# Performance work log

Hardware: AMD Instinct MI355X
Metric: run time of the kernel (lower is better)

Reference implementation:

```python
import jax, jax.numpy as jnp
import numpy as np

DIM = 1024
DIM_LATENT = 1024
DIM_HEAD = 64
INNER = max(DIM, DIM_LATENT)  # 1024
HEADS = INNER // DIM_HEAD     # 16
SCALE = DIM_HEAD ** -0.5
LN_EPS = 1e-5
RMS_EPS = 1e-8


def layernorm(x, g, b):
    mu = jnp.mean(x, axis=-1, keepdims=True)
    var = jnp.mean(jnp.square(x - mu), axis=-1, keepdims=True)
    return (x - mu) * jax.lax.rsqrt(var + LN_EPS) * g + b


def rmsnorm(x, gamma):
    # torch: x / clamp(norm(x,-1) * d**-0.5, eps) * gamma
    n = jnp.linalg.norm(x, axis=-1, keepdims=True) * (x.shape[-1] ** -0.5)
    return x / jnp.maximum(n, RMS_EPS) * gamma


def setup_inputs() -> dict:
    key = jax.random.key(0)
    ks = jax.random.split(key, 8)
    b, n, nl = 8, 2048, 512
    x = jax.random.normal(ks[0], (b, n, DIM), dtype=jnp.float32)
    latents = jax.random.normal(ks[1], (b, nl, DIM_LATENT), dtype=jnp.float32)
    mask = jax.random.randint(ks[2], (b, n), 0, 2).astype(bool)
    init = lambda k, shape, fan_in: jax.random.normal(k, shape, jnp.float32) * (fan_in ** -0.5)
    return {
        "x": x,
        "latents": latents,
        "mask": mask,
        "ln_x_g": jnp.ones((DIM,), jnp.float32),
        "ln_x_b": jnp.zeros((DIM,), jnp.float32),
        "ln_l_g": jnp.ones((DIM_LATENT,), jnp.float32),
        "ln_l_b": jnp.zeros((DIM_LATENT,), jnp.float32),
        "q_gamma": jnp.ones((DIM_HEAD,), jnp.float32),
        "k_gamma": jnp.ones((DIM_HEAD,), jnp.float32),
        "W_q": init(ks[3], (DIM_LATENT, INNER), DIM_LATENT),
        "W_kv": init(ks[4], (DIM, 2 * INNER), DIM),
        "W_out": init(ks[5], (INNER, DIM_LATENT), INNER),
        "b_out": jnp.zeros((DIM_LATENT,), jnp.float32),
    }


def reference(x, latents, mask, ln_x_g, ln_x_b, ln_l_g, ln_l_b,
              q_gamma, k_gamma, W_q, W_kv, W_out, b_out):
    b, n, _ = x.shape
    nl = latents.shape[1]
    xn = layernorm(x, ln_x_g, ln_x_b)
    ln = layernorm(latents, ln_l_g, ln_l_b)

    q = ln @ W_q                                   # [b, nl, inner]
    kv = jnp.concatenate([xn @ W_kv, ln @ W_kv], axis=1)  # [b, n+nl, 2*inner]
    k, v = kv[..., :INNER], kv[..., INNER:]

    to_heads = lambda t: t.reshape(t.shape[0], t.shape[1], HEADS, DIM_HEAD).transpose(0, 2, 1, 3)
    q, k, v = to_heads(q), to_heads(k), to_heads(v)  # [b, h, *, d]

    qn = rmsnorm(q, q_gamma) * SCALE
    kn = rmsnorm(k, k_gamma)

    sim = jnp.einsum('bhid,bhjd->bhij', qn, kn)      # [b, h, nl, n+nl]
    full_mask = jnp.pad(mask, ((0, 0), (0, nl)), constant_values=True)
    neg = -jnp.finfo(sim.dtype).max
    sim = jnp.where(full_mask[:, None, None, :], sim, neg)

    attn = jax.nn.softmax(sim.astype(jnp.float32), axis=-1).astype(sim.dtype)
    out = jnp.einsum('bhij,bhjd->bhid', attn, v)     # [b, h, nl, d]
    out = out.transpose(0, 2, 1, 3).reshape(b, nl, INNER)
    return out @ W_out + b_out
```

## Files before the change

kernel.cpp:

```cpp
#include <hip/hip_runtime.h>
#include <hip/hip_bf16.h>
#include <cfloat>
#include <cmath>

typedef __hip_bfloat16 bf16;
#define DEV_INLINE __device__ __forceinline__

typedef __attribute__((ext_vector_type(8))) short short8;
typedef __attribute__((ext_vector_type(4))) short short4v;
typedef __attribute__((ext_vector_type(4))) float float4v;
typedef __attribute__((ext_vector_type(16))) float float16v;

#define BATCH 8
#define NSEQ 2048
#define NLAT 512
#define DIM_ 1024
#define NKV 2560
#define HEADS_ 16
#define DHEAD 64
#define SCALE_ 0.125f
#define LN_EPS_ 1e-5f
#define RMS_EPS_ 1e-8f

DEV_INLINE float bf2f(bf16 v) { return __bfloat162float(v); }
DEV_INLINE bf16 f2bf(float v) { return __float2bfloat16(v); }
DEV_INLINE short bfbits(float x) { union { bf16 b; short s; } c; c.b = f2bf(x); return c.s; }
DEV_INLINE float sbits2f(short s) { union { bf16 b; short s; } c; c.s = s; return bf2f(c.b); }

DEV_INLINE int detect_bf16(const void* ones) {
    return (*(const unsigned*)ones == 0x3F803F80u) ? 1 : 0;
}

template<typename T> DEV_INLINE float ldf(const T* p);
template<> DEV_INLINE float ldf<float>(const float* p) { return *p; }
template<> DEV_INLINE float ldf<bf16>(const bf16* p)  { return __bfloat162float(*p); }

DEV_INLINE void gload16(const bf16* g, bf16* l) {
    __builtin_amdgcn_global_load_lds(
        (const __attribute__((address_space(1))) unsigned int*)g,
        (__attribute__((address_space(3))) unsigned int*)l,
        16, 0, 0);
}

DEV_INLINE float block_sum_256(float v, float* sred) {
    #pragma unroll
    for (int o = 1; o < 64; o <<= 1) v += __shfl_xor(v, o, 64);
    int w = threadIdx.x >> 6;
    __syncthreads();
    if ((threadIdx.x & 63) == 0) sred[w] = v;
    __syncthreads();
    return sred[0] + sred[1] + sred[2] + sred[3];
}

template<typename T>
DEV_INLINE void ln_row_body(int r, const void* xv, const void* latv,
                            const void* gxv, const void* bxv,
                            const void* glv, const void* blv,
                            bf16* __restrict__ out, float* sred)
{
    const T* src; const T* g; const T* be; bf16* o;
    if (r < BATCH * NSEQ) {
        int b = r >> 11, i = r & 2047;
        src = (const T*)xv + (size_t)r * DIM_;
        o = out + ((size_t)b * NKV + i) * DIM_;
        g = (const T*)gxv; be = (const T*)bxv;
    } else {
        int rr = r - BATCH * NSEQ;
        int b = rr >> 9, i = rr & 511;
        src = (const T*)latv + (size_t)rr * DIM_;
        o = out + ((size_t)b * NKV + NSEQ + i) * DIM_;
        g = (const T*)glv; be = (const T*)blv;
    }
    int t = threadIdx.x;
    float v[4];
    float s = 0.f;
    #pragma unroll
    for (int j = 0; j < 4; j++) { v[j] = ldf(src + t + j * 256); s += v[j]; }
    s = block_sum_256(s, sred);
    float mu = s * (1.f / 1024.f);
    float s2 = 0.f;
    #pragma unroll
    for (int j = 0; j < 4; j++) { float d = v[j] - mu; s2 += d * d; }
    s2 = block_sum_256(s2, sred);
    float rstd = rsqrtf(s2 * (1.f / 1024.f) + LN_EPS_);
    #pragma unroll
    for (int j = 0; j < 4; j++) {
        int c = t + j * 256;
        o[c] = f2bf((v[j] - mu) * rstd * ldf(g + c) + ldf(be + c));
    }
}

template<typename T>
DEV_INLINE void trans_body(int bid, const void* wqv, const void* wkvv, const void* woutv,
                           bf16* wqT, bf16* wkvT, bf16* woutT, float* tile )
{
    const T* in; bf16* out; int N, t0;
    if (bid < 1024)      { in = (const T*)wqv;   out = wqT;   N = 1024; t0 = bid; }
    else if (bid < 3072) { in = (const T*)wkvv;  out = wkvT;  N = 2048; t0 = bid - 1024; }
    else                 { in = (const T*)woutv; out = woutT; N = 1024; t0 = bid - 3072; }
    int K = 1024;
    int nb = N >> 5;
    int bn = (t0 % nb) * 32, bk = (t0 / nb) * 32;
    int tx = threadIdx.x & 31, ty = threadIdx.x >> 5;
    #pragma unroll
    for (int j = 0; j < 4; j++)
        tile[(ty + j * 8) * 33 + tx] = ldf(in + (size_t)(bk + ty + j * 8) * N + bn + tx);
    __syncthreads();
    #pragma unroll
    for (int j = 0; j < 4; j++)
        out[(size_t)(bn + ty + j * 8) * K + bk + tx] = f2bf(tile[tx * 33 + ty + j * 8]);
}

__global__ __launch_bounds__(256) void prep_kernel(
    const void* x, const void* lat,
    const void* gx, const void* bx, const void* gl, const void* bl,
    const void* wq, const void* wkv, const void* wout,
    bf16* __restrict__ cat_n, bf16* __restrict__ wqT,
    bf16* __restrict__ wkvT, bf16* __restrict__ woutT)
{
    __shared__ float smem[32 * 33];
    int isb = detect_bf16(gx);
    int bid = blockIdx.x;
    if (bid < 20480) {
        if (isb) ln_row_body<bf16>(bid, x, lat, gx, bx, gl, bl, cat_n, smem);
        else     ln_row_body<float>(bid, x, lat, gx, bx, gl, bl, cat_n, smem);
    } else {
        int t = bid - 20480;
        if (isb) trans_body<bf16>(t, wq, wkv, wout, wqT, wkvT, woutT, smem);
        else     trans_body<float>(t, wq, wkv, wout, wqT, wkvT, woutT, smem);
    }
}

#define MFMA_CORE_128(As, Bs, Apt, Bpt, K, acc)                                \
    {                                                                          \
        bf16* Asl_ = &As[threadIdx.x * 8];                                     \
        bf16* Bsl_ = &Bs[threadIdx.x * 8];                                     \
        for (int k0 = 0; k0 < K; k0 += 64) {                                   \
            __syncthreads();                                                   \
            _Pragma("unroll")                                                  \
            for (int rep = 0; rep < 4; rep++) {                                \
                gload16(Apt[rep] + k0, Asl_ + rep * 2048);                     \
                gload16(Bpt[rep] + k0, Bsl_ + rep * 2048);                     \
            }                                                                  \
            __syncthreads();                                                   \
            _Pragma("unroll")                                                  \
            for (int kk = 0; kk < 4; kk++) {                                   \
                short8 af_[2], bf_[2];                                         \
                _Pragma("unroll")                                              \
                for (int ms = 0; ms < 2; ms++) {                               \
                    int row = wm * 64 + ms * 32 + l32;                         \
                    int jc = (kk * 2 + h5) ^ (row & 7);                        \
                    af_[ms] = *(const short8*)&As[row * 64 + jc * 8];          \
                }                                                              \
                _Pragma("unroll")                                              \
                for (int ns = 0; ns < 2; ns++) {                               \
                    int row = wn * 64 + ns * 32 + l32;                         \
                    int jc = (kk * 2 + h5) ^ (row & 7);                        \
                    bf_[ns] = *(const short8*)&Bs[row * 64 + jc * 8];          \
                }                                                              \
                _Pragma("unroll")                                              \
                for (int ms = 0; ms < 2; ms++)                                 \
                    _Pragma("unroll")                                          \
                    for (int ns = 0; ns < 2; ns++)                             \
                        acc[ms][ns] = __builtin_amdgcn_mfma_f32_32x32x16_bf16( \
                            af_[ms], bf_[ns], acc[ms][ns], 0, 0, 0);           \
            }                                                                  \
        }                                                                      \
    }

#define QKV_MFMA2(BQ0, BQ1, NB)                                               \
    __builtin_amdgcn_s_barrier(); asm volatile("" ::: "memory");              \
    __builtin_amdgcn_s_setprio(1);                                            \
    _Pragma("unroll")                                                         \
    for (int m_ = 0; m_ < 8; m_++) {                                          \
        acc[m_][NB] = __builtin_amdgcn_mfma_f32_16x16x32_bf16(                \
            af[m_], BQ0, acc[m_][NB], 0, 0, 0);                               \
        acc[m_][NB + 1] = __builtin_amdgcn_mfma_f32_16x16x32_bf16(            \
            af[m_], BQ1, acc[m_][NB + 1], 0, 0, 0);                           \
    }                                                                         \
    __builtin_amdgcn_s_setprio(0);                                            \
    __builtin_amdgcn_s_barrier(); asm volatile("" ::: "memory");

__global__ __launch_bounds__(512, 2) void gemm_qkv(
    const void* gq, const void* gk,
    const bf16* __restrict__ cat_n, const bf16* __restrict__ wkvT,
    const bf16* __restrict__ wqT,
    bf16* __restrict__ kbuf, bf16* __restrict__ vtbuf, bf16* __restrict__ qbuf)
{
    __shared__ bf16 S[8][8192];
    int isb = detect_bf16(gq);
    int tid = threadIdx.x;
    int bid = blockIdx.x;
    int lane = tid & 63;
    int l16 = lane & 15, quad = lane >> 4;
    int wv = tid >> 6;
    int wm = wv >> 2, wn = wv & 3;

    int x = bid & 7, ii = bid >> 3;
    int bm, bn; bool isq; const bf16* Bt;
    if (ii < 80) { bm = (ii >> 3) * 8 + x; bn = ii & 7; Bt = wkvT; isq = false; }
    else { int j = ii - 80; bm = (j >> 2) * 8 + x; bn = j & 3; Bt = wqT; isq = true; }

    int r0 = tid >> 2;
    int c0 = (tid & 3) ^ ((r0 >> 1) & 3);
    int r1 = (tid + 512) >> 2;
    int c1 = (tid & 3) ^ ((r1 >> 1) & 3);
    int ar0 = bm * 256 + r0, ar1 = bm * 256 + r1;
    size_t ga0 = isq ? ((size_t)(ar0 >> 9) * NKV + NSEQ + (ar0 & 511)) : (size_t)ar0;
    size_t ga1 = isq ? ((size_t)(ar1 >> 9) * NKV + NSEQ + (ar1 & 511)) : (size_t)ar1;
    const bf16* pA0 = cat_n + ga0 * 1024 + c0 * 8;
    const bf16* pA1 = cat_n + ga1 * 1024 + c1 * 8;
    const bf16* pB0 = Bt + (size_t)(bn * 256 + r0) * 1024 + c0 * 8;
    const bf16* pB1 = Bt + (size_t)(bn * 256 + r1) * 1024 + c1 * 8;

#define STG(P0, P1, SLOT, KO) do {                                            \
        gload16((P0) + (KO), &S[SLOT][0] + tid * 8);                          \
        gload16((P1) + (KO), &S[SLOT][0] + 4096 + tid * 8);                   \
    } while (0)

    int qx = (quad ^ ((l16 >> 1) & 3)) * 8;
    int aoff = (wm * 128 + l16) * 32 + qx;
    int boff = (wn * 64 + l16) * 32 + qx;

    float4v acc[8][4];
    #pragma unroll
    for (int m = 0; m < 8; m++)
        #pragma unroll
        for (int n = 0; n < 4; n++)
            #pragma unroll
            for (int r = 0; r < 4; r++) acc[m][n][r] = 0.f;

    STG(pA0, pA1, 0, 0);
    STG(pB0, pB1, 2, 0);
    STG(pA0, pA1, 1, 32);
    STG(pB0, pB1, 3, 32);
    STG(pA0, pA1, 4, 64);
    STG(pB0, pB1, 6, 64);
    asm volatile("s_waitcnt vmcnt(4)" ::: "memory");
    __builtin_amdgcn_s_barrier(); asm volatile("" ::: "memory");

    short8 af[8], b0[4], b1[4];
    b0[0] = *(const short8*)&S[2][boff];
    b0[1] = *(const short8*)&S[2][boff + 512];

    for (int t = 0; t < 16; ++t) {
        int cur = (t & 1) * 4, nxt = cur ^ 4;
        const bf16* A0k = &S[cur + 0][0];
        const bf16* A1k = &S[cur + 1][0];
        const bf16* B0k = &S[cur + 2][0];
        const bf16* B1k = &S[cur + 3][0];
        const bf16* Bn0 = &S[nxt + 2][0];
        int ko1 = t * 64 + 96;
        int ko2 = t * 64 + 128;

        #pragma unroll
        for (int m = 0; m < 8; m++) af[m] = *(const short8*)&A0k[aoff + m * 512];
        if (t < 15) STG(pA0, pA1, nxt + 1, ko1);
        QKV_MFMA2(b0[0], b0[1], 0)

        b0[2] = *(const short8*)&B0k[boff + 1024];
        b0[3] = *(const short8*)&B0k[boff + 1536];
        b1[0] = *(const short8*)&B1k[boff];
        b1[1] = *(const short8*)&B1k[boff + 512];
        if (t < 15) STG(pB0, pB1, nxt + 3, ko1);
        QKV_MFMA2(b0[2], b0[3], 2)

        #pragma unroll
        for (int m = 0; m < 8; m++) af[m] = *(const short8*)&A1k[aoff + m * 512];
        if (t < 14) STG(pA0, pA1, cur + 0, ko2);
        QKV_MFMA2(b1[0], b1[1], 0)

        b1[2] = *(const short8*)&B1k[boff + 1024];
        b1[3] = *(const short8*)&B1k[boff + 1536];
        if (t < 14) {
            STG(pB0, pB1, cur + 2, ko2);
            asm volatile("s_waitcnt vmcnt(4)" ::: "memory");
        } else {
            asm volatile("s_waitcnt vmcnt(0)" ::: "memory");
        }
        if (t < 15) {
            b0[0] = *(const short8*)&Bn0[boff];
            b0[1] = *(const short8*)&Bn0[boff + 512];
        }
        QKV_MFMA2(b1[2], b1[3], 2)
    }
#undef STG

    if (isq || bn < 4) {
        const void* gp = isq ? gq : gk;
        float g2[4];
        #pragma unroll
        for (int n = 0; n < 4; n++) {
            int idx = n * 16 + l16;
            g2[n] = isb ? bf2f(((const bf16*)gp)[idx]) : ((const float*)gp)[idx];
        }
        #pragma unroll
        for (int m = 0; m < 8; m++) {
            #pragma unroll
            for (int r = 0; r < 4; r++) {
                float ss = acc[m][0][r] * acc[m][0][r]
                         + acc[m][1][r] * acc[m][1][r]
                         + acc[m][2][r] * acc[m][2][r]
                         + acc[m][3][r] * acc[m][3][r];
                ss += __shfl_xor(ss, 1, 64);
                ss += __shfl_xor(ss, 2, 64);
                ss += __shfl_xor(ss, 4, 64);
                ss += __shfl_xor(ss, 8, 64);
                float nn = sqrtf(ss) * 0.125f;
                float inv = 1.0f / fmaxf(nn, RMS_EPS_);
                if (isq) inv *= SCALE_;
                #pragma unroll
                for (int n = 0; n < 4; n++) acc[m][n][r] *= inv * g2[n];
            }
        }
    }

    if (!isq && bn >= 4) {
        int bq_ = bm / 10;
        int key0 = (bm % 10) * 256 + wm * 128;
        #pragma unroll
        for (int m = 0; m < 8; m++) {
            int key = key0 + m * 16 + quad * 4;
            #pragma unroll
            for (int n = 0; n < 4; n++) {
                int col = bn * 256 + wn * 64 + n * 16 + l16 - 1024;
                int h = col >> 6, d = col & 63;
                short4v ov;
                #pragma unroll
                for (int r = 0; r < 4; r++) ov[r] = bfbits(acc[m][n][r]);
                *(short4v*)(vtbuf + ((size_t)((bq_ * 16 + h) * 64 + d)) * NKV + key) = ov;
            }
        }
    } else {
        bf16* C = isq ? qbuf : kbuf;
        int rbase = bm * 256 + wm * 128;
        int cbase = bn * 256 + wn * 64;
        #pragma unroll
        for (int m = 0; m < 8; m++) {
            #pragma unroll
            for (int r = 0; r < 4; r++) {
                int row = rbase + m * 16 + quad * 4 + r;
                #pragma unroll
                for (int n = 0; n < 4; n++)
                    C[(size_t)row * 1024 + cbase + n * 16 + l16] = f2bf(acc[m][n][r]);
            }
        }
    }
}

#define KC 64
__global__ __launch_bounds__(256) void attn_mfma(
    const bf16* __restrict__ q, const bf16* __restrict__ kbuf,
    const bf16* __restrict__ vtbuf, const int* __restrict__ maskp,
    const void* gk, bf16* __restrict__ out)
{
    __shared__ bf16 Ks[KC * 64];
    __shared__ bf16 Vt[DHEAD * 64];
    __shared__ bf16 Ps[4][2][16][64];
    __shared__ float msk_s[KC];

    int isb = detect_bf16(gk);
    int tid = threadIdx.x;
    int bid = blockIdx.x;
    int bh = bid & 127, qb = bid >> 7;
    int h = bh & 15, bb = bh >> 4;
    int wv = tid >> 6, lane = tid & 63, quad = lane >> 4, l16 = lane & 15;
    int q8 = quad * 8;
    int qbase = qb * 128 + wv * 32;
    int sw = l16 & 7;

    const bf16* kbase = kbuf + (size_t)bb * NKV * 1024 + h * DHEAD;
    const bf16* vbase = vtbuf + (size_t)(bb * 16 + h) * DHEAD * NKV;

    short8 qf[2][2];
    #pragma unroll
    for (int qt = 0; qt < 2; qt++) {
        const bf16* qp = q + ((size_t)(bb * NLAT + qbase + qt * 16 + l16)) * 1024 + h * DHEAD;
        qf[qt][0] = *(const short8*)(qp + q8);
        qf[qt][1] = *(const short8*)(qp + q8 + 32);
    }

    float gv = isb ? bf2f(((const bf16*)gk)[lane]) : ((const float*)gk)[lane];
    gv = fabsf(gv);
    #pragma unroll
    for (int o = 1; o < 64; o <<= 1) gv = fmaxf(gv, __shfl_xor(gv, o, 64));
    float m_fix[2];
    #pragma unroll
    for (int qt = 0; qt < 2; qt++) {
        float ssq = 0.f;
        #pragma unroll
        for (int j = 0; j < 8; j++) {
            float a = sbits2f(qf[qt][0][j]);
            float b = sbits2f(qf[qt][1][j]);
            ssq += a * a + b * b;
        }
        ssq += __shfl_xor(ssq, 16, 64);
        ssq += __shfl_xor(ssq, 32, 64);
        m_fix[qt] = sqrtf(ssq) * 8.0f * gv;
    }

    int c0 = tid, c1 = tid + 256;
    int krow0 = c0 >> 3, kj0 = ((c0 & 7) ^ (krow0 & 7)) * 8;
    int krow1 = c1 >> 3, kj1 = ((c1 & 7) ^ (krow1 & 7)) * 8;

    float4v o_acc[2][4];
    #pragma unroll
    for (int qt = 0; qt < 2; qt++)
        #pragma unroll
        for (int ds = 0; ds < 4; ds++)
            #pragma unroll
            for (int r = 0; r < 4; r++) o_acc[qt][ds][r] = 0.f;
    float l_i[2] = {0.f, 0.f};

    for (int kb = 0; kb < NKV; kb += KC) {
        __syncthreads();
        gload16(kbase + (size_t)(kb + krow0) * 1024 + kj0, &Ks[c0 * 8]);
        gload16(kbase + (size_t)(kb + krow1) * 1024 + kj1, &Ks[c1 * 8]);
        gload16(vbase + (size_t)krow0 * NKV + kb + kj0, &Vt[c0 * 8]);
        gload16(vbase + (size_t)krow1 * NKV + kb + kj1, &Vt[c1 * 8]);
        if (tid < KC) {
            int key = kb + tid;
            float mv = 0.f;
            if (key < NSEQ) mv = maskp[bb * NSEQ + key] ? 0.f : -1e30f;
            msk_s[tid] = mv;
        }
        __syncthreads();

        float4v st[2][4];
        #pragma unroll
        for (int kt = 0; kt < 4; kt++) {
            int row = kt * 16 + l16;
            short8 kf0 = *(const short8*)&Ks[row * 64 + ((quad ^ sw) << 3)];
            short8 kf1 = *(const short8*)&Ks[row * 64 + (((quad + 4) ^ sw) << 3)];
            #pragma unroll
            for (int qt = 0; qt < 2; qt++) {
                float4v z; z[0]=0.f; z[1]=0.f; z[2]=0.f; z[3]=0.f;
                z = __builtin_amdgcn_mfma_f32_16x16x32_bf16(kf0, qf[qt][0], z, 0, 0, 0);
                z = __builtin_amdgcn_mfma_f32_16x16x32_bf16(kf1, qf[qt][1], z, 0, 0, 0);
                st[qt][kt] = z;
            }
        }
        float4 mv4[4];
        #pragma unroll
        for (int kt = 0; kt < 4; kt++) mv4[kt] = *(const float4*)&msk_s[kt * 16 + 4 * quad];
        #pragma unroll
        for (int qt = 0; qt < 2; qt++) {
            float lp = 0.f;
            #pragma unroll
            for (int kt = 0; kt < 4; kt++) {
                const float* mk = (const float*)&mv4[kt];
                short4v pk;
                #pragma unroll
                for (int r = 0; r < 4; r++) {
                    float e = __expf(st[qt][kt][r] + mk[r] - m_fix[qt]);
                    lp += e;
                    pk[r] = bfbits(e);
                }
                int j = kt * 2 + (quad >> 1);
                int js = j ^ sw;
                *(short4v*)&Ps[wv][qt][l16][js * 8 + (quad & 1) * 4] = pk;
            }
            l_i[qt] += lp;
        }

        #pragma unroll
        for (int kc = 0; kc < 2; kc++) {
            short8 pf[2];
            #pragma unroll
            for (int qt = 0; qt < 2; qt++)
                pf[qt] = *(const short8*)&Ps[wv][qt][l16][((kc * 4 + quad) ^ sw) * 8];
            #pragma unroll
            for (int ds = 0; ds < 4; ds++) {
                int row = ds * 16 + l16;
                short8 vf = *(const short8*)&Vt[row * 64 + (((kc * 4 + quad) ^ sw) << 3)];
                #pragma unroll
                for (int qt = 0; qt < 2; qt++)
                    o_acc[qt][ds] = __builtin_amdgcn_mfma_f32_16x16x32_bf16(vf, pf[qt], o_acc[qt][ds], 0, 0, 0);
            }
        }
    }

    #pragma unroll
    for (int qt = 0; qt < 2; qt++) {
        float l = l_i[qt];
        l += __shfl_xor(l, 16, 64);
        l += __shfl_xor(l, 32, 64);
        float inv = 1.0f / l;
        bf16* op = out + ((size_t)(bb * NLAT + qbase + qt * 16 + l16)) * 1024 + h * DHEAD;
        #pragma unroll
        for (int ds = 0; ds < 4; ds++) {
            short4v ov;
            #pragma unroll
            for (int r = 0; r < 4; r++) ov[r] = bfbits(o_acc[qt][ds][r] * inv);
            *(short4v*)(op + ds * 16 + 4 * quad) = ov;
        }
    }
}

__global__ __launch_bounds__(256) void gemm_out(
    const void* ones, const void* bias,
    const bf16* __restrict__ A, const bf16* __restrict__ Bt, void* __restrict__ Cout)
{
    __shared__ bf16 As[128 * 64];
    __shared__ bf16 Bs[128 * 64];
    int isb = detect_bf16(ones);

    int tid = threadIdx.x;
    int bid = blockIdx.x;
    int bm = (bid >> 6) * 8 + (bid & 7);
    int bn = (bid >> 3) & 7;
    int wv = tid >> 6, lane = tid & 63, l32 = lane & 31, h5 = lane >> 5;
    int wm = wv >> 1, wn = wv & 1;
    const int K = 1024, N = 1024;

    const bf16* Apt[4]; const bf16* Bpt[4];
    #pragma unroll
    for (int rep = 0; rep < 4; rep++) {
        int c = rep * 256 + tid;
        int row = c >> 3;
        int k8 = ((c & 7) ^ (row & 7)) * 8;
        Apt[rep] = A + (size_t)(bm * 128 + row) * K + k8;
        Bpt[rep] = Bt + (size_t)(bn * 128 + row) * K + k8;
    }

    float16v acc[2][2];
    #pragma unroll
    for (int i = 0; i < 2; i++)
        #pragma unroll
        for (int j = 0; j < 2; j++)
            #pragma unroll
            for (int r = 0; r < 16; r++) acc[i][j][r] = 0.f;

    MFMA_CORE_128(As, Bs, Apt, Bpt, K, acc);

    #pragma unroll
    for (int ms = 0; ms < 2; ms++) {
        #pragma unroll
        for (int rg = 0; rg < 4; rg++) {
            int row0 = bm * 128 + wm * 64 + ms * 32 + rg * 8 + h5 * 4;
            #pragma unroll
            for (int rr = 0; rr < 4; rr++) {
                int row = row0 + rr;
                #pragma unroll
                for (int ns = 0; ns < 2; ns++) {
                    int col = bn * 128 + wn * 64 + ns * 32 + l32;
                    float bv = isb ? bf2f(((const bf16*)bias)[col]) : ((const float*)bias)[col];
                    float v = acc[ms][ns][rg * 4 + rr] + bv;
                    if (isb) ((bf16*)Cout)[(size_t)row * N + col] = f2bf(v);
                    else     ((float*)Cout)[(size_t)row * N + col] = v;
                }
            }
        }
    }
}

extern "C" void kernel_launch(void* const* d_in, const int* in_sizes, int n_in,
                              void* d_out, int out_size, void* d_ws, size_t ws_size,
                              hipStream_t stream) {
    const int* mask = (const int*)d_in[2];

    char* ws = (char*)d_ws;
    size_t off = 0;
    bf16* cat_n   = (bf16*)(ws + off); off += (size_t)20480 * 1024 * 2;
    bf16* kbuf    = (bf16*)(ws + off); off += (size_t)20480 * 1024 * 2;
    bf16* vtbuf   = (bf16*)(ws + off); off += (size_t)8192 * 2560 * 2;
    bf16* qbuf    = (bf16*)(ws + off); off += (size_t)4096 * 1024 * 2;
    bf16* attnout = (bf16*)(ws + off); off += (size_t)4096 * 1024 * 2;
    bf16* wqT     = (bf16*)(ws + off); off += (size_t)1024 * 1024 * 2;
    bf16* wkvT    = (bf16*)(ws + off); off += (size_t)2048 * 1024 * 2;
    bf16* woutT   = (bf16*)(ws + off); off += (size_t)1024 * 1024 * 2;

    prep_kernel<<<24576, 256, 0, stream>>>(
        d_in[0], d_in[1], d_in[3], d_in[4], d_in[5], d_in[6],
        d_in[9], d_in[10], d_in[11], cat_n, wqT, wkvT, woutT);

    gemm_qkv<<<704, 512, 0, stream>>>(
        d_in[7], d_in[8], cat_n, wkvT, wqT, kbuf, vtbuf, qbuf);

    attn_mfma<<<512, 256, 0, stream>>>(qbuf, kbuf, vtbuf, mask, d_in[8], attnout);

    gemm_out<<<256, 256, 0, stream>>>(
        d_in[3], d_in[12], attnout, woutT, d_out);
}
```

Measured before the change: 357.5 us.

## Double-buffer K/V tiles in attention, preload mask, restructure QKV MFMA clusters

The attention kernel now double-buffers the K and V shared-memory tiles, issuing the next tile's global loads before computing on the current one, and drops one barrier per iteration. The full mask row is converted into shared memory once up front instead of per tile. The QKV GEMM loads all four B fragments at once and runs two larger MFMA clusters per k-step, with an explicit lgkmcnt wait and sched_barrier, instead of four smaller interleaved ones. This uses more LDS and registers and makes the waits coarser, so it could lower occupancy or expose LDS latency.

```diff
diff --git a/kernel.cpp b/kernel.cpp
--- a/kernel.cpp
+++ b/kernel.cpp
@@ -168,16 +168,17 @@
         }                                                                      \
     }
 
-#define QKV_MFMA2(BQ0, BQ1, NB)                                               \
+#define QKV_CLUSTER()                                                         \
     __builtin_amdgcn_s_barrier(); asm volatile("" ::: "memory");              \
+    asm volatile("s_waitcnt lgkmcnt(0)" ::: "memory");                        \
+    __builtin_amdgcn_sched_barrier(0);                                        \
     __builtin_amdgcn_s_setprio(1);                                            \
     _Pragma("unroll")                                                         \
-    for (int m_ = 0; m_ < 8; m_++) {                                          \
-        acc[m_][NB] = __builtin_amdgcn_mfma_f32_16x16x32_bf16(                \
-            af[m_], BQ0, acc[m_][NB], 0, 0, 0);                               \
-        acc[m_][NB + 1] = __builtin_amdgcn_mfma_f32_16x16x32_bf16(            \
-            af[m_], BQ1, acc[m_][NB + 1], 0, 0, 0);                           \
-    }                                                                         \
+    for (int m_ = 0; m_ < 8; m_++)                                            \
+        _Pragma("unroll")                                                     \
+        for (int n_ = 0; n_ < 4; n_++)                                        \
+            acc[m_][n_] = __builtin_amdgcn_mfma_f32_16x16x32_bf16(            \
+                af[m_], bfr[n_], acc[m_][n_], 0, 0, 0);                       \
     __builtin_amdgcn_s_setprio(0);                                            \
     __builtin_amdgcn_s_barrier(); asm volatile("" ::: "memory");
 
@@ -239,50 +240,38 @@
     asm volatile("s_waitcnt vmcnt(4)" ::: "memory");
     __builtin_amdgcn_s_barrier(); asm volatile("" ::: "memory");
 
-    short8 af[8], b0[4], b1[4];
-    b0[0] = *(const short8*)&S[2][boff];
-    b0[1] = *(const short8*)&S[2][boff + 512];
-
+    short8 af[8], bfr[4];
     for (int t = 0; t < 16; ++t) {
         int cur = (t & 1) * 4, nxt = cur ^ 4;
         const bf16* A0k = &S[cur + 0][0];
         const bf16* A1k = &S[cur + 1][0];
         const bf16* B0k = &S[cur + 2][0];
         const bf16* B1k = &S[cur + 3][0];
-        const bf16* Bn0 = &S[nxt + 2][0];
         int ko1 = t * 64 + 96;
         int ko2 = t * 64 + 128;
 
         #pragma unroll
         for (int m = 0; m < 8; m++) af[m] = *(const short8*)&A0k[aoff + m * 512];
-        if (t < 15) STG(pA0, pA1, nxt + 1, ko1);
-        QKV_MFMA2(b0[0], b0[1], 0)
-
-        b0[2] = *(const short8*)&B0k[boff + 1024];
-        b0[3] = *(const short8*)&B0k[boff + 1536];
-        b1[0] = *(const short8*)&B1k[boff];
-        b1[1] = *(const short8*)&B1k[boff + 512];
-        if (t < 15) STG(pB0, pB1, nxt + 3, ko1);
-        QKV_MFMA2(b0[2], b0[3], 2)
+        #pragma unroll
+        for (int n = 0; n < 4; n++) bfr[n] = *(const short8*)&B0k[boff + n * 512];
+        if (t < 15) {
+            STG(pA0, pA1, nxt + 1, ko1);
+            STG(pB0, pB1, nxt + 3, ko1);
+        }
+        QKV_CLUSTER()
 
         #pragma unroll
         for (int m = 0; m < 8; m++) af[m] = *(const short8*)&A1k[aoff + m * 512];
-        if (t < 14) STG(pA0, pA1, cur + 0, ko2);
-        QKV_MFMA2(b1[0], b1[1], 0)
-
-        b1[2] = *(const short8*)&B1k[boff + 1024];
-        b1[3] = *(const short8*)&B1k[boff + 1536];
+        #pragma unroll
+        for (int n = 0; n < 4; n++) bfr[n] = *(const short8*)&B1k[boff + n * 512];
         if (t < 14) {
+            STG(pA0, pA1, cur + 0, ko2);
             STG(pB0, pB1, cur + 2, ko2);
             asm volatile("s_waitcnt vmcnt(4)" ::: "memory");
         } else {
             asm volatile("s_waitcnt vmcnt(0)" ::: "memory");
         }
-        if (t < 15) {
-            b0[0] = *(const short8*)&Bn0[boff];
-            b0[1] = *(const short8*)&Bn0[boff + 512];
-        }
-        QKV_MFMA2(b1[2], b1[3], 2)
+        QKV_CLUSTER()
     }
 #undef STG
 
@@ -354,10 +343,10 @@
     const bf16* __restrict__ vtbuf, const int* __restrict__ maskp,
     const void* gk, bf16* __restrict__ out)
 {
-    __shared__ bf16 Ks[KC * 64];
-    __shared__ bf16 Vt[DHEAD * 64];
+    __shared__ bf16 Ks[2][KC * 64];
+    __shared__ bf16 Vt[2][DHEAD * 64];
     __shared__ bf16 Ps[4][2][16][64];
-    __shared__ float msk_s[KC];
+    __shared__ float msk_all[NSEQ];
 
     int isb = detect_bf16(gk);
     int tid = threadIdx.x;
@@ -372,6 +361,12 @@
     const bf16* kbase = kbuf + (size_t)bb * NKV * 1024 + h * DHEAD;
     const bf16* vbase = vtbuf + (size_t)(bb * 16 + h) * DHEAD * NKV;
 
+    #pragma unroll
+    for (int j = 0; j < 8; j++) {
+        int key = j * 256 + tid;
+        msk_all[key] = maskp[bb * NSEQ + key] ? 0.f : -1e30f;
+    }
+
     short8 qf[2][2];
     #pragma unroll
     for (int qt = 0; qt < 2; qt++) {
@@ -399,9 +394,16 @@
         m_fix[qt] = sqrtf(ssq) * 8.0f * gv;
     }
 
-    int c0 = tid, c1 = tid + 256;
-    int krow0 = c0 >> 3, kj0 = ((c0 & 7) ^ (krow0 & 7)) * 8;
-    int krow1 = c1 >> 3, kj1 = ((c1 & 7) ^ (krow1 & 7)) * 8;
+    int sc0 = tid, sc1 = tid + 256;
+    int krow0 = sc0 >> 3, kj0 = ((sc0 & 7) ^ (krow0 & 7)) * 8;
+    int krow1 = sc1 >> 3, kj1 = ((sc1 & 7) ^ (krow1 & 7)) * 8;
+
+#define ASTG(B, KB) do {                                                      \
+        gload16(kbase + (size_t)((KB) + krow0) * 1024 + kj0, &Ks[B][sc0 * 8]);\
+        gload16(kbase + (size_t)((KB) + krow1) * 1024 + kj1, &Ks[B][sc1 * 8]);\
+        gload16(vbase + (size_t)krow0 * NKV + (KB) + kj0, &Vt[B][sc0 * 8]);   \
+        gload16(vbase + (size_t)krow1 * NKV + (KB) + kj1, &Vt[B][sc1 * 8]);   \
+    } while (0)
 
     float4v o_acc[2][4];
     #pragma unroll
@@ -412,26 +414,19 @@
             for (int r = 0; r < 4; r++) o_acc[qt][ds][r] = 0.f;
     float l_i[2] = {0.f, 0.f};
 
+    ASTG(0, 0);
+    __syncthreads();
+
+    int buf = 0;
     for (int kb = 0; kb < NKV; kb += KC) {
-        __syncthreads();
-        gload16(kbase + (size_t)(kb + krow0) * 1024 + kj0, &Ks[c0 * 8]);
-        gload16(kbase + (size_t)(kb + krow1) * 1024 + kj1, &Ks[c1 * 8]);
-        gload16(vbase + (size_t)krow0 * NKV + kb + kj0, &Vt[c0 * 8]);
-        gload16(vbase + (size_t)krow1 * NKV + kb + kj1, &Vt[c1 * 8]);
-        if (tid < KC) {
-            int key = kb + tid;
-            float mv = 0.f;
-            if (key < NSEQ) mv = maskp[bb * NSEQ + key] ? 0.f : -1e30f;
-            msk_s[tid] = mv;
-        }
-        __syncthreads();
+        if (kb + KC < NKV) ASTG(buf ^ 1, kb + KC);
 
         float4v st[2][4];
         #pragma unroll
         for (int kt = 0; kt < 4; kt++) {
             int row = kt * 16 + l16;
-            short8 kf0 = *(const short8*)&Ks[row * 64 + ((quad ^ sw) << 3)];
-            short8 kf1 = *(const short8*)&Ks[row * 64 + (((quad + 4) ^ sw) << 3)];
+            short8 kf0 = *(const short8*)&Ks[buf][row * 64 + ((quad ^ sw) << 3)];
+            short8 kf1 = *(const short8*)&Ks[buf][row * 64 + (((quad + 4) ^ sw) << 3)];
             #pragma unroll
             for (int qt = 0; qt < 2; qt++) {
                 float4v z; z[0]=0.f; z[1]=0.f; z[2]=0.f; z[3]=0.f;
@@ -441,8 +436,15 @@
             }
         }
         float4 mv4[4];
-        #pragma unroll
-        for (int kt = 0; kt < 4; kt++) mv4[kt] = *(const float4*)&msk_s[kt * 16 + 4 * quad];
+        if (kb < NSEQ) {
+            #pragma unroll
+            for (int kt = 0; kt < 4; kt++)
+                mv4[kt] = *(const float4*)&msk_all[kb + kt * 16 + 4 * quad];
+        } else {
+            #pragma unroll
+            for (int kt = 0; kt < 4; kt++)
+                mv4[kt] = make_float4(0.f, 0.f, 0.f, 0.f);
+        }
         #pragma unroll
         for (int qt = 0; qt < 2; qt++) {
             float lp = 0.f;
@@ -472,13 +474,17 @@
             #pragma unroll
             for (int ds = 0; ds < 4; ds++) {
                 int row = ds * 16 + l16;
-                short8 vf = *(const short8*)&Vt[row * 64 + (((kc * 4 + quad) ^ sw) << 3)];
+                short8 vf = *(const short8*)&Vt[buf][row * 64 + (((kc * 4 + quad) ^ sw) << 3)];
                 #pragma unroll
                 for (int qt = 0; qt < 2; qt++)
                     o_acc[qt][ds] = __builtin_amdgcn_mfma_f32_16x16x32_bf16(vf, pf[qt], o_acc[qt][ds], 0, 0, 0);
             }
         }
-    }
+
+        __syncthreads();
+        buf ^= 1;
+    }
+#undef ASTG
 
     #pragma unroll
     for (int qt = 0; qt < 2; qt++) {
```

New measurement: 370.5 us. 1.04x slower.

## Switch QKV GEMM to 32x32x16 MFMA with simpler double-buffered pipeline

Applied to the files above, without the earlier changes.

The QKV projection GEMM moves from 16x16x32 MFMA tiles to 32x32x16 MFMA tiles, so each wave holds a 4x2 grid of 16-float accumulators instead of 8x4 float4s. The staggered four-phase prefetch with partial vmcnt waits and barriers around every MFMA group is replaced by a plain double buffer: prefetch the whole next k-tile, compute both halves, then wait and barrier once per iteration. The RMSNorm and store epilogues are remapped to the new accumulator layout, adding one more shuffle step. Larger MFMAs reduce LDS fragment reads per FLOP, but the simpler pipeline may expose more global-load latency.

```diff
diff --git a/kernel.cpp b/kernel.cpp
--- a/kernel.cpp
+++ b/kernel.cpp
@@ -168,19 +168,6 @@
         }                                                                      \
     }
 
-#define QKV_MFMA2(BQ0, BQ1, NB)                                               \
-    __builtin_amdgcn_s_barrier(); asm volatile("" ::: "memory");              \
-    __builtin_amdgcn_s_setprio(1);                                            \
-    _Pragma("unroll")                                                         \
-    for (int m_ = 0; m_ < 8; m_++) {                                          \
-        acc[m_][NB] = __builtin_amdgcn_mfma_f32_16x16x32_bf16(                \
-            af[m_], BQ0, acc[m_][NB], 0, 0, 0);                               \
-        acc[m_][NB + 1] = __builtin_amdgcn_mfma_f32_16x16x32_bf16(            \
-            af[m_], BQ1, acc[m_][NB + 1], 0, 0, 0);                           \
-    }                                                                         \
-    __builtin_amdgcn_s_setprio(0);                                            \
-    __builtin_amdgcn_s_barrier(); asm volatile("" ::: "memory");
-
 __global__ __launch_bounds__(512, 2) void gemm_qkv(
     const void* gq, const void* gk,
     const bf16* __restrict__ cat_n, const bf16* __restrict__ wkvT,
@@ -192,7 +179,7 @@
     int tid = threadIdx.x;
     int bid = blockIdx.x;
     int lane = tid & 63;
-    int l16 = lane & 15, quad = lane >> 4;
+    int l32 = lane & 31, h5 = lane >> 5;
     int wv = tid >> 6;
     int wm = wv >> 2, wn = wv & 3;
 
@@ -218,30 +205,30 @@
         gload16((P1) + (KO), &S[SLOT][0] + 4096 + tid * 8);                   \
     } while (0)
 
-    int qx = (quad ^ ((l16 >> 1) & 3)) * 8;
-    int aoff = (wm * 128 + l16) * 32 + qx;
-    int boff = (wn * 64 + l16) * 32 + qx;
-
-    float4v acc[8][4];
-    #pragma unroll
-    for (int m = 0; m < 8; m++)
-        #pragma unroll
-        for (int n = 0; n < 4; n++)
-            #pragma unroll
-            for (int r = 0; r < 4; r++) acc[m][n][r] = 0.f;
+    int ax = (l32 >> 1) & 3;
+    int ch[2];
+    ch[0] = ((h5) ^ ax) * 8;
+    ch[1] = ((2 + h5) ^ ax) * 8;
+    int arow[4], brow[2];
+    #pragma unroll
+    for (int mi = 0; mi < 4; mi++) arow[mi] = (wm * 128 + mi * 32 + l32) * 32;
+    #pragma unroll
+    for (int ni = 0; ni < 2; ni++) brow[ni] = (wn * 64 + ni * 32 + l32) * 32;
+
+    float16v acc[4][2];
+    #pragma unroll
+    for (int mi = 0; mi < 4; mi++)
+        #pragma unroll
+        for (int ni = 0; ni < 2; ni++)
+            #pragma unroll
+            for (int r = 0; r < 16; r++) acc[mi][ni][r] = 0.f;
 
     STG(pA0, pA1, 0, 0);
+    STG(pA0, pA1, 1, 32);
     STG(pB0, pB1, 2, 0);
-    STG(pA0, pA1, 1, 32);
     STG(pB0, pB1, 3, 32);
-    STG(pA0, pA1, 4, 64);
-    STG(pB0, pB1, 6, 64);
-    asm volatile("s_waitcnt vmcnt(4)" ::: "memory");
+    asm volatile("s_waitcnt vmcnt(0)" ::: "memory");
     __builtin_amdgcn_s_barrier(); asm volatile("" ::: "memory");
-
-    short8 af[8], b0[4], b1[4];
-    b0[0] = *(const short8*)&S[2][boff];
-    b0[1] = *(const short8*)&S[2][boff + 512];
 
     for (int t = 0; t < 16; ++t) {
         int cur = (t & 1) * 4, nxt = cur ^ 4;
@@ -249,68 +236,89 @@
         const bf16* A1k = &S[cur + 1][0];
         const bf16* B0k = &S[cur + 2][0];
         const bf16* B1k = &S[cur + 3][0];
-        const bf16* Bn0 = &S[nxt + 2][0];
-        int ko1 = t * 64 + 96;
-        int ko2 = t * 64 + 128;
-
-        #pragma unroll
-        for (int m = 0; m < 8; m++) af[m] = *(const short8*)&A0k[aoff + m * 512];
-        if (t < 15) STG(pA0, pA1, nxt + 1, ko1);
-        QKV_MFMA2(b0[0], b0[1], 0)
-
-        b0[2] = *(const short8*)&B0k[boff + 1024];
-        b0[3] = *(const short8*)&B0k[boff + 1536];
-        b1[0] = *(const short8*)&B1k[boff];
-        b1[1] = *(const short8*)&B1k[boff + 512];
-        if (t < 15) STG(pB0, pB1, nxt + 3, ko1);
-        QKV_MFMA2(b0[2], b0[3], 2)
-
-        #pragma unroll
-        for (int m = 0; m < 8; m++) af[m] = *(const short8*)&A1k[aoff + m * 512];
-        if (t < 14) STG(pA0, pA1, cur + 0, ko2);
-        QKV_MFMA2(b1[0], b1[1], 0)
-
-        b1[2] = *(const short8*)&B1k[boff + 1024];
-        b1[3] = *(const short8*)&B1k[boff + 1536];
-        if (t < 14) {
-            STG(pB0, pB1, cur + 2, ko2);
-            asm volatile("s_waitcnt vmcnt(4)" ::: "memory");
-        } else {
-            asm volatile("s_waitcnt vmcnt(0)" ::: "memory");
-        }
+
         if (t < 15) {
-            b0[0] = *(const short8*)&Bn0[boff];
-            b0[1] = *(const short8*)&Bn0[boff + 512];
-        }
-        QKV_MFMA2(b1[2], b1[3], 2)
+            int ko = (t + 1) * 64;
+            STG(pA0, pA1, nxt + 0, ko);
+            STG(pA0, pA1, nxt + 1, ko + 32);
+            STG(pB0, pB1, nxt + 2, ko);
+            STG(pB0, pB1, nxt + 3, ko + 32);
+        }
+        __builtin_amdgcn_sched_barrier(0);
+
+        short8 a0[4][2], b0[2][2];
+        #pragma unroll
+        for (int mi = 0; mi < 4; mi++) {
+            a0[mi][0] = *(const short8*)&A0k[arow[mi] + ch[0]];
+            a0[mi][1] = *(const short8*)&A0k[arow[mi] + ch[1]];
+        }
+        #pragma unroll
+        for (int ni = 0; ni < 2; ni++) {
+            b0[ni][0] = *(const short8*)&B0k[brow[ni] + ch[0]];
+            b0[ni][1] = *(const short8*)&B0k[brow[ni] + ch[1]];
+        }
+        __builtin_amdgcn_s_setprio(1);
+        #pragma unroll
+        for (int s = 0; s < 2; s++)
+            #pragma unroll
+            for (int mi = 0; mi < 4; mi++)
+                #pragma unroll
+                for (int ni = 0; ni < 2; ni++)
+                    acc[mi][ni] = __builtin_amdgcn_mfma_f32_32x32x16_bf16(
+                        a0[mi][s], b0[ni][s], acc[mi][ni], 0, 0, 0);
+        __builtin_amdgcn_s_setprio(0);
+
+        short8 a1[4][2], b1[2][2];
+        #pragma unroll
+        for (int mi = 0; mi < 4; mi++) {
+            a1[mi][0] = *(const short8*)&A1k[arow[mi] + ch[0]];
+            a1[mi][1] = *(const short8*)&A1k[arow[mi] + ch[1]];
+        }
+        #pragma unroll
+        for (int ni = 0; ni < 2; ni++) {
+            b1[ni][0] = *(const short8*)&B1k[brow[ni] + ch[0]];
+            b1[ni][1] = *(const short8*)&B1k[brow[ni] + ch[1]];
+        }
+        __builtin_amdgcn_s_setprio(1);
+        #pragma unroll
+        for (int s = 0; s < 2; s++)
+            #pragma unroll
+            for (int mi = 0; mi < 4; mi++)
+                #pragma unroll
+                for (int ni = 0; ni < 2; ni++)
+                    acc[mi][ni] = __builtin_amdgcn_mfma_f32_32x32x16_bf16(
+                        a1[mi][s], b1[ni][s], acc[mi][ni], 0, 0, 0);
+        __builtin_amdgcn_s_setprio(0);
+
+        asm volatile("s_waitcnt vmcnt(0)" ::: "memory");
+        __builtin_amdgcn_s_barrier(); asm volatile("" ::: "memory");
     }
 #undef STG
 
     if (isq || bn < 4) {
         const void* gp = isq ? gq : gk;
-        float g2[4];
-        #pragma unroll
-        for (int n = 0; n < 4; n++) {
-            int idx = n * 16 + l16;
-            g2[n] = isb ? bf2f(((const bf16*)gp)[idx]) : ((const float*)gp)[idx];
-        }
-        #pragma unroll
-        for (int m = 0; m < 8; m++) {
-            #pragma unroll
-            for (int r = 0; r < 4; r++) {
-                float ss = acc[m][0][r] * acc[m][0][r]
-                         + acc[m][1][r] * acc[m][1][r]
-                         + acc[m][2][r] * acc[m][2][r]
-                         + acc[m][3][r] * acc[m][3][r];
+        float g2[2];
+        #pragma unroll
+        for (int ni = 0; ni < 2; ni++) {
+            int idx = ni * 32 + l32;
+            g2[ni] = isb ? bf2f(((const bf16*)gp)[idx]) : ((const float*)gp)[idx];
+        }
+        #pragma unroll
+        for (int mi = 0; mi < 4; mi++) {
+            #pragma unroll
+            for (int rg = 0; rg < 16; rg++) {
+                float ss = acc[mi][0][rg] * acc[mi][0][rg]
+                         + acc[mi][1][rg] * acc[mi][1][rg];
                 ss += __shfl_xor(ss, 1, 64);
                 ss += __shfl_xor(ss, 2, 64);
                 ss += __shfl_xor(ss, 4, 64);
                 ss += __shfl_xor(ss, 8, 64);
+                ss += __shfl_xor(ss, 16, 64);
                 float nn = sqrtf(ss) * 0.125f;
                 float inv = 1.0f / fmaxf(nn, RMS_EPS_);
                 if (isq) inv *= SCALE_;
-                #pragma unroll
-                for (int n = 0; n < 4; n++) acc[m][n][r] *= inv * g2[n];
+                acc[mi][0][rg] *= inv * g2[0];
+                acc[mi][1][rg] *= inv * g2[1];
             }
         }
     }
@@ -319,30 +327,37 @@
         int bq_ = bm / 10;
         int key0 = (bm % 10) * 256 + wm * 128;
         #pragma unroll
-        for (int m = 0; m < 8; m++) {
-            int key = key0 + m * 16 + quad * 4;
-            #pragma unroll
-            for (int n = 0; n < 4; n++) {
-                int col = bn * 256 + wn * 64 + n * 16 + l16 - 1024;
-                int h = col >> 6, d = col & 63;
-                short4v ov;
-                #pragma unroll
-                for (int r = 0; r < 4; r++) ov[r] = bfbits(acc[m][n][r]);
-                *(short4v*)(vtbuf + ((size_t)((bq_ * 16 + h) * 64 + d)) * NKV + key) = ov;
+        for (int mi = 0; mi < 4; mi++) {
+            #pragma unroll
+            for (int rg = 0; rg < 4; rg++) {
+                int key = key0 + mi * 32 + rg * 8 + h5 * 4;
+                #pragma unroll
+                for (int ni = 0; ni < 2; ni++) {
+                    int col = bn * 256 + wn * 64 + ni * 32 + l32 - 1024;
+                    int h = col >> 6, d = col & 63;
+                    short4v ov;
+                    #pragma unroll
+                    for (int rr = 0; rr < 4; rr++) ov[rr] = bfbits(acc[mi][ni][rg * 4 + rr]);
+                    *(short4v*)(vtbuf + ((size_t)((bq_ * 16 + h) * 64 + d)) * NKV + key) = ov;
+                }
             }
         }
     } else {
         bf16* C = isq ? qbuf : kbuf;
-        int rbase = bm * 256 + wm * 128;
-        int cbase = bn * 256 + wn * 64;
-        #pragma unroll
-        for (int m = 0; m < 8; m++) {
-            #pragma unroll
-            for (int r = 0; r < 4; r++) {
-                int row = rbase + m * 16 + quad * 4 + r;
-                #pragma unroll
-                for (int n = 0; n < 4; n++)
-                    C[(size_t)row * 1024 + cbase + n * 16 + l16] = f2bf(acc[m][n][r]);
+        #pragma unroll
+        for (int mi = 0; mi < 4; mi++) {
+            #pragma unroll
+            for (int rg = 0; rg < 4; rg++) {
+                int row0 = bm * 256 + wm * 128 + mi * 32 + rg * 8 + h5 * 4;
+                #pragma unroll
+                for (int rr = 0; rr < 4; rr++) {
+                    int row = row0 + rr;
+                    #pragma unroll
+                    for (int ni = 0; ni < 2; ni++) {
+                        int col = bn * 256 + wn * 64 + ni * 32 + l32;
+                        C[(size_t)row * 1024 + col] = f2bf(acc[mi][ni][rg * 4 + rr]);
+                    }
+                }
             }
         }
     }
```

Result: slower. 377.5 us (+5.6%).
